# Kernel tuning notes

Hardware: AMD Instinct MI355X
Metric: run time of the kernel (lower is better)

Reference implementation:

```python
import jax, jax.numpy as jnp
import numpy as np

# Model dims (match init_kwargs)
B, S = 2, 2048          # batch, seq_len
H = 1024                # hidden_size
D = 2048                # expert_hidden_dim
E = 8                   # num_experts
K = 2                   # num_experts_per_tok (top_k)


def setup_inputs() -> dict:
    key = jax.random.key(0)
    k_x, k_g, k_w1, k_w2 = jax.random.split(key, 4)
    x = jax.random.normal(k_x, (B, S, H), jnp.float32)
    # router gate: Linear(H, E, bias=False)
    gate_w = jax.random.normal(k_g, (H, E), jnp.float32) / jnp.sqrt(H).astype(jnp.float32)
    # per-expert FFN params stacked on leading expert axis
    W1 = jax.random.normal(k_w1, (E, H, D), jnp.float32) / jnp.sqrt(H).astype(jnp.float32)
    b1 = jnp.zeros((E, D), jnp.float32)
    W2 = jax.random.normal(k_w2, (E, D, H), jnp.float32) / jnp.sqrt(D).astype(jnp.float32)
    b2 = jnp.zeros((E, H), jnp.float32)
    return {"x": x, "gate_w": gate_w, "W1": W1, "b1": b1, "W2": W2, "b2": b2}


def reference(x, gate_w, W1, b1, W2, b2):
    # --- router ---
    logits = jnp.einsum('bsh,he->bse', x, gate_w)            # [B,S,E]
    probs = jax.nn.softmax(logits, axis=-1)                  # [B,S,E]
    topk_p, idx = jax.lax.top_k(probs, K)                    # [B,S,K] each
    topk_p = topk_p / topk_p.sum(axis=-1, keepdims=True)     # renormalize over top-k
    one_hot = jax.nn.one_hot(idx, E, dtype=probs.dtype)      # [B,S,K,E]
    # combine weight per (token, expert); topk indices are distinct so this
    # equals the original's masked-sum of router_probs_flat * expert_mask
    combine = jnp.einsum('bske,bsk->bse', one_hot, topk_p)   # [B,S,E]

    # --- aux load-balancing loss (faithful to original reductions) ---
    tokens_per_expert = one_hot.sum(axis=-2).mean(axis=0)    # [S,E]
    avg_prob_per_expert = probs.mean(axis=(0, 1))            # [E]
    aux_loss = E * (tokens_per_expert * avg_prob_per_expert).sum()

    # --- experts: dense-equivalent of gather-FFN-scatter (tokens with
    # combine weight 0 contribute 0, matching the masked loop) ---
    out = jnp.zeros_like(x)
    for e in range(E):  # fixed small loop over structurally distinct experts
        h = jax.nn.gelu(jnp.einsum('bsh,hd->bsd', x, W1[e]) + b1[e], approximate=False)
        out = out + combine[..., e:e + 1] * (jnp.einsum('bsd,dh->bsh', h, W2[e]) + b2[e])
    return out, aux_loss
```

## Files before the change

### kernel.cpp

```cpp
#include <hip/hip_runtime.h>
#include <hip/hip_bf16.h>

#define NTOK 4096
#define HD   1024
#define DD   2048
#define NE   8
#define SLOTS (2*NTOK)
#define SLOTS_PAD (SLOTS + 128)

typedef unsigned short u16;
typedef unsigned int   u32;
typedef __attribute__((ext_vector_type(8))) __bf16 bf16x8;
typedef __attribute__((ext_vector_type(4))) float  f32x4;

__device__ __forceinline__ float bf2f(u16 u) {
    u32 v = ((u32)u) << 16;
    return __uint_as_float(v);
}
__device__ __forceinline__ u16 f2bf(float f) {
    __hip_bfloat16 h = __float2bfloat16(f);
    return *reinterpret_cast<u16*>(&h);
}

__device__ __forceinline__ void gload_lds16(const void* g, void* l) {
    __builtin_amdgcn_global_load_lds(
        (__attribute__((address_space(1))) void*)g,
        (__attribute__((address_space(3))) void*)l,
        16, 0, 0);
}

__global__ __launch_bounds__(256) void cvt2_k(
        const float* __restrict__ W1, const float* __restrict__ W2,
        u16* __restrict__ W1t, u16* __restrict__ W2t) {
    int z = blockIdx.z;
    const float* src; u16* dst; int R, C;
    if (z < NE) { src = W1 + (size_t)z * HD * DD;        dst = W1t + (size_t)z * HD * DD;        R = HD; C = DD; }
    else        { src = W2 + (size_t)(z - NE) * DD * HD; dst = W2t + (size_t)(z - NE) * DD * HD; R = DD; C = HD; }
    int tcols = C >> 6;
    int r0 = (blockIdx.x / tcols) * 64;
    int c0 = (blockIdx.x % tcols) * 64;

    __shared__ u16 tile[64][68];
    int tid = threadIdx.x;
    int rr  = tid >> 4;
    int cc4 = (tid & 15) * 4;
#pragma unroll
    for (int j = 0; j < 4; ++j) {
        int r = rr + j * 16;
        float4 v = *reinterpret_cast<const float4*>(src + (size_t)(r0 + r) * C + c0 + cc4);
        tile[r][cc4 + 0] = f2bf(v.x); tile[r][cc4 + 1] = f2bf(v.y);
        tile[r][cc4 + 2] = f2bf(v.z); tile[r][cc4 + 3] = f2bf(v.w);
    }
    __syncthreads();
    int cc = tid >> 3, sl = tid & 7;
#pragma unroll
    for (int p = 0; p < 2; ++p) {
        int c = p * 32 + cc;
        u16 tmp[8];
#pragma unroll
        for (int k = 0; k < 8; ++k) tmp[k] = tile[sl * 8 + k][c];
        *reinterpret_cast<uint4*>(dst + (size_t)(c0 + c) * R + r0 + sl * 8) =
            *reinterpret_cast<uint4*>(tmp);
    }
}

__global__ __launch_bounds__(256) void router_k(
        const float* __restrict__ x, const float* __restrict__ gw,
        u16* __restrict__ xb,
        int* __restrict__ counts, float* __restrict__ sum_probs,
        int* __restrict__ tk_idx, float* __restrict__ tk_w) {
    __shared__ int   bcnt[NE];
    __shared__ float bprob[NE];
    int tid = threadIdx.x;
    if (tid < NE) { bcnt[tid] = 0; bprob[tid] = 0.f; }
    __syncthreads();

    int gtid = blockIdx.x * 256 + tid;
    int t    = gtid >> 6;
    int lane = gtid & 63;

    float acc[NE] = {0.f,0.f,0.f,0.f,0.f,0.f,0.f,0.f};
    const float* xr = x + (size_t)t * HD;
    u16* xbr = xb + (size_t)t * HD;
#pragma unroll
    for (int i = 0; i < HD / 64; ++i) {
        int h = lane + i * 64;
        float xv = xr[h];
        xbr[h] = f2bf(xv);
        const float4* g = reinterpret_cast<const float4*>(gw + (size_t)h * NE);
        float4 g0 = g[0], g1 = g[1];
        acc[0] = fmaf(xv, g0.x, acc[0]); acc[1] = fmaf(xv, g0.y, acc[1]);
        acc[2] = fmaf(xv, g0.z, acc[2]); acc[3] = fmaf(xv, g0.w, acc[3]);
        acc[4] = fmaf(xv, g1.x, acc[4]); acc[5] = fmaf(xv, g1.y, acc[5]);
        acc[6] = fmaf(xv, g1.z, acc[6]); acc[7] = fmaf(xv, g1.w, acc[7]);
    }
#pragma unroll
    for (int off = 32; off >= 1; off >>= 1) {
#pragma unroll
        for (int e = 0; e < NE; ++e) acc[e] += __shfl_xor(acc[e], off);
    }
    float m = acc[0];
#pragma unroll
    for (int e = 1; e < NE; ++e) m = fmaxf(m, acc[e]);
    float p[NE]; float s = 0.f;
#pragma unroll
    for (int e = 0; e < NE; ++e) { p[e] = expf(acc[e] - m); s += p[e]; }
    float inv = 1.f / s;

    int i1 = 0; float v1 = p[0];
#pragma unroll
    for (int e = 1; e < NE; ++e) if (p[e] > v1) { v1 = p[e]; i1 = e; }
    int i2 = -1; float v2 = -1.f;
#pragma unroll
    for (int e = 0; e < NE; ++e) if (e != i1 && p[e] > v2) { v2 = p[e]; i2 = e; }
    float wsum = v1 + v2;

    if (lane < NE) atomicAdd(&bprob[lane], p[lane] * inv);
    if (lane == 0) {
        atomicAdd(&bcnt[i1], 1);
        atomicAdd(&bcnt[i2], 1);
        tk_idx[2 * t]     = i1;  tk_idx[2 * t + 1] = i2;
        tk_w[2 * t]       = v1 / wsum;
        tk_w[2 * t + 1]   = v2 / wsum;
    }
    __syncthreads();
    if (tid < NE) {
        if (bcnt[tid]) atomicAdd(&counts[tid], bcnt[tid]);
        atomicAdd(&sum_probs[tid], bprob[tid]);
    }
}

__global__ __launch_bounds__(256) void scatter_k(
        const int* __restrict__ tk_idx, const int* __restrict__ counts,
        int* __restrict__ cursor, int* __restrict__ slot_tok,
        int* __restrict__ inv_slot, int* __restrict__ offsets) {
    __shared__ int off[NE];
    if (threadIdx.x == 0) {
        int o = 0;
        for (int e = 0; e < NE; ++e) { off[e] = o; o += counts[e]; }
        if (blockIdx.x == 0)
            for (int e = 0; e < NE; ++e) offsets[e] = off[e];
    }
    __syncthreads();
    int t = blockIdx.x * 256 + threadIdx.x;
    if (t >= NTOK) return;
#pragma unroll
    for (int k = 0; k < 2; ++k) {
        int e = tk_idx[2 * t + k];
        int pos = atomicAdd(&cursor[e], 1);
        int s = off[e] + pos;
        slot_tok[s] = t;
        inv_slot[2 * t + k] = s;
    }
}

template<int KD, bool GATHER, bool GELU>
__global__ __launch_bounds__(256) void gemm_dense_k(
        const u16* __restrict__ A,
        const u16* __restrict__ Bt,
        const float* __restrict__ bias,
        const int* __restrict__ counts, const int* __restrict__ offsets,
        const int* __restrict__ slot_tok,
        u16* __restrict__ outb, int ND) {
    int mb = blockIdx.y;
    int e = -1, m0 = 0, accb = 0;
#pragma unroll
    for (int ee = 0; ee < NE; ++ee) {
        int nb = (counts[ee] + 127) >> 7;
        if (e < 0 && mb < accb + nb) { e = ee; m0 = (mb - accb) * 128; }
        accb += nb;
    }
    if (e < 0) return;
    int cnt = counts[e], base = offsets[e];
    int n0 = blockIdx.x * 128;

    __shared__ u16 As[128 * 64];
    __shared__ u16 Bs[128 * 64];
    __shared__ int ids[128];

    int tid  = threadIdx.x;
    int lane = tid & 63;
    int w    = tid >> 6;
    int wr   = w >> 1, wc = w & 1;
    int lrow = lane & 15, khi = lane >> 4;

    if constexpr (GATHER) {
        if (tid < 128) ids[tid] = (m0 + tid < cnt) ? slot_tok[base + m0 + tid] : 0;
    }
    __syncthreads();

    const u16* Bte = Bt + (size_t)e * (size_t)ND * KD;
    int srow = tid >> 3;
    int sslot = tid & 7;

    const u16 *gA[4], *gB[4];
#pragma unroll
    for (int j = 0; j < 4; ++j) {
        int r = j * 32 + srow;
        size_t gr;
        if constexpr (GATHER) gr = (size_t)ids[r];
        else                  gr = (size_t)(base + m0 + r);
        gA[j] = A   + gr * KD                + ((sslot ^ (r & 7)) << 3);
        gB[j] = Bte + (size_t)(n0 + r) * KD  + ((sslot ^ (r & 7)) << 3);
    }

    f32x4 acc[4][4];
#pragma unroll
    for (int m = 0; m < 4; ++m)
#pragma unroll
        for (int n = 0; n < 4; ++n) acc[m][n] = {0.f, 0.f, 0.f, 0.f};

    constexpr int NK = KD / 64;
#pragma unroll 1
    for (int t = 0; t < NK; ++t) {
#pragma unroll
        for (int j = 0; j < 4; ++j) {
            gload_lds16(gA[j] + t * 64, (char*)As + j * 4096 + tid * 16);
            gload_lds16(gB[j] + t * 64, (char*)Bs + j * 4096 + tid * 16);
        }
        __syncthreads();
#pragma unroll
        for (int ks = 0; ks < 2; ++ks) {
            int slot = ks * 4 + khi;
            bf16x8 af[4], bv[4];
#pragma unroll
            for (int m = 0; m < 4; ++m) {
                int r = wr * 64 + m * 16 + lrow;
                af[m] = *reinterpret_cast<const bf16x8*>(
                    &As[r * 64 + ((slot ^ (r & 7)) << 3)]);
            }
#pragma unroll
            for (int n = 0; n < 4; ++n) {
                int r = wc * 64 + n * 16 + lrow;
                bv[n] = *reinterpret_cast<const bf16x8*>(
                    &Bs[r * 64 + ((slot ^ (r & 7)) << 3)]);
            }
            __builtin_amdgcn_s_setprio(1);
#pragma unroll
            for (int m = 0; m < 4; ++m)
#pragma unroll
                for (int n = 0; n < 4; ++n)
                    acc[m][n] = __builtin_amdgcn_mfma_f32_16x16x32_bf16(
                        af[m], bv[n], acc[m][n], 0, 0, 0);
            __builtin_amdgcn_s_setprio(0);
        }
        __syncthreads();
    }

    constexpr int PST = 72;
    u16* patch = As + w * 16 * PST;
    float bvals[4];
    if constexpr (GELU) {
#pragma unroll
        for (int n = 0; n < 4; ++n)
            bvals[n] = bias[(size_t)e * ND + n0 + wc * 64 + n * 16 + lrow];
    }
#pragma unroll
    for (int m = 0; m < 4; ++m) {
#pragma unroll
        for (int n = 0; n < 4; ++n)
#pragma unroll
            for (int i = 0; i < 4; ++i) {
                float v = acc[m][n][i];
                if constexpr (GELU) {
                    v += bvals[n];
                    v = 0.5f * v * (1.f + erff(v * 0.70710678118654752f));
                }
                patch[(khi * 4 + i) * PST + n * 16 + lrow] = f2bf(v);
            }
        __syncthreads();
        int prow = lane >> 3, sl = lane & 7;
#pragma unroll
        for (int p = 0; p < 2; ++p) {
            int row  = p * 8 + prow;
            uint4 q = *reinterpret_cast<const uint4*>(&patch[row * PST + sl * 8]);
            int grow = m0 + wr * 64 + m * 16 + row;
            if (grow < cnt)
                *reinterpret_cast<uint4*>(
                    outb + (size_t)(base + grow) * ND + n0 + wc * 64 + sl * 8) = q;
        }
        __syncthreads();
    }
}

__global__ __launch_bounds__(256) void combine_k(
        const int* __restrict__ tk_idx, const float* __restrict__ tk_w,
        const int* __restrict__ inv_slot, const u16* __restrict__ ybuf,
        const float* __restrict__ b2, float* __restrict__ out) {
    int gtid = blockIdx.x * 256 + threadIdx.x;
    int t = gtid >> 6;
    int lane = gtid & 63;
    int e0 = tk_idx[2 * t], e1 = tk_idx[2 * t + 1];
    float w0 = tk_w[2 * t], w1 = tk_w[2 * t + 1];
    int s0 = inv_slot[2 * t], s1 = inv_slot[2 * t + 1];

#pragma unroll
    for (int i = 0; i < 2; ++i) {
        int c = lane * 8 + i * 512;
        uint4 q0 = *reinterpret_cast<const uint4*>(ybuf + (size_t)s0 * HD + c);
        uint4 q1 = *reinterpret_cast<const uint4*>(ybuf + (size_t)s1 * HD + c);
        float y0[8] = {bf2f((u16)(q0.x&0xffff)), bf2f((u16)(q0.x>>16)),
                       bf2f((u16)(q0.y&0xffff)), bf2f((u16)(q0.y>>16)),
                       bf2f((u16)(q0.z&0xffff)), bf2f((u16)(q0.z>>16)),
                       bf2f((u16)(q0.w&0xffff)), bf2f((u16)(q0.w>>16))};
        float y1[8] = {bf2f((u16)(q1.x&0xffff)), bf2f((u16)(q1.x>>16)),
                       bf2f((u16)(q1.y&0xffff)), bf2f((u16)(q1.y>>16)),
                       bf2f((u16)(q1.z&0xffff)), bf2f((u16)(q1.z>>16)),
                       bf2f((u16)(q1.w&0xffff)), bf2f((u16)(q1.w>>16))};
        float r[8];
#pragma unroll
        for (int j = 0; j < 8; ++j) {
            float v0 = y0[j] + b2[e0 * HD + c + j];
            float v1 = y1[j] + b2[e1 * HD + c + j];
            r[j] = w0 * v0 + w1 * v1;
        }
        float* op = out + (size_t)t * HD + c;
        *reinterpret_cast<float4*>(op)     = make_float4(r[0], r[1], r[2], r[3]);
        *reinterpret_cast<float4*>(op + 4) = make_float4(r[4], r[5], r[6], r[7]);
    }
}

__global__ void finalize_k(const int* __restrict__ counts,
                           const float* __restrict__ sum_probs,
                           float* __restrict__ out_aux) {
    if (threadIdx.x == 0) {
        double s = 0.0;
        for (int e = 0; e < NE; ++e) s += (double)counts[e] * (double)sum_probs[e];
        out_aux[0] = (float)(s * (8.0 / (2.0 * (double)NTOK)));
    }
}

extern "C" void kernel_launch(void* const* d_in, const int* in_sizes, int n_in,
                              void* d_out, int out_size, void* d_ws, size_t ws_size,
                              hipStream_t stream) {
    const float* x   = (const float*)d_in[0];
    const float* gw  = (const float*)d_in[1];
    const float* W1  = (const float*)d_in[2];
    const float* b1  = (const float*)d_in[3];
    const float* W2  = (const float*)d_in[4];
    const float* b2  = (const float*)d_in[5];
    float* out = (float*)d_out;

    char* ws = (char*)d_ws;
    int*   counts    = (int*)(ws + 0);
    int*   cursor    = (int*)(ws + 32);
    int*   offsets   = (int*)(ws + 64);
    float* sum_probs = (float*)(ws + 128);
    int*   tk_idx    = (int*)(ws + 512);
    float* tk_w      = (float*)(ws + 33280);
    int*   slot_tok  = (int*)(ws + 66048);
    int*   inv_slot  = (int*)(ws + 98816);
    u16*   xb        = (u16*)(ws + 131584);
    u16*   W1t       = (u16*)(ws + 8520192);
    u16*   W2t       = (u16*)(ws + 42074624);
    u16*   hbuf      = (u16*)(ws + 75629056);
    u16*   ybuf      = W1t;

    hipMemsetAsync(ws, 0, 512, stream);

    cvt2_k<<<dim3(512, 1, 2 * NE), 256, 0, stream>>>(W1, W2, W1t, W2t);
    router_k<<<NTOK / 4, 256, 0, stream>>>(x, gw, xb, counts, sum_probs, tk_idx, tk_w);
    scatter_k<<<NTOK / 256, 256, 0, stream>>>(tk_idx, counts, cursor,
                                              slot_tok, inv_slot, offsets);

    gemm_dense_k<HD, true, true><<<dim3(DD / 128, 72, 1), 256, 0, stream>>>(
        xb, W1t, b1, counts, offsets, slot_tok, hbuf, DD);
    gemm_dense_k<DD, false, false><<<dim3(HD / 128, 72, 1), 256, 0, stream>>>(
        hbuf, W2t, nullptr, counts, offsets, slot_tok, ybuf, HD);

    combine_k<<<NTOK / 4, 256, 0, stream>>>(tk_idx, tk_w, inv_slot, ybuf, b2, out);
    finalize_k<<<1, 64, 0, stream>>>(counts, sum_probs, out + (size_t)NTOK * HD);
}
```

Before: 220.9 us.

## Rewrite expert GEMM as 256x256 tile, 8-wave double-buffered pipelined kernel

Replaces the 128x128 single-buffered grouped GEMM with a 256x256 tile kernel using 8 waves and a double-buffered LDS ring. Global-to-LDS loads for the next k-tile are interleaved with four quadrant MFMA phases under explicit vmcnt/lgkmcnt waits and barriers. This aims to hide memory latency and raise data reuse per loaded tile. In exchange it uses 128KB of LDS, fewer and larger blocks (more padding waste per expert), and carries fragile hand-tuned wait counts.

```diff
diff --git a/kernel.cpp b/kernel.cpp
--- a/kernel.cpp
+++ b/kernel.cpp
@@ -6,12 +6,19 @@
 #define DD   2048
 #define NE   8
 #define SLOTS (2*NTOK)
-#define SLOTS_PAD (SLOTS + 128)
+#define SLOTS_PAD (SLOTS + 256)
 
 typedef unsigned short u16;
 typedef unsigned int   u32;
 typedef __attribute__((ext_vector_type(8))) __bf16 bf16x8;
 typedef __attribute__((ext_vector_type(4))) float  f32x4;
+
+#define WAITV(N) asm volatile("s_waitcnt vmcnt(" #N ")" ::: "memory")
+#define LGKM0()  asm volatile("s_waitcnt lgkmcnt(0)" ::: "memory")
+#define BAR()    __builtin_amdgcn_s_barrier()
+#define SCHEDB() __builtin_amdgcn_sched_barrier(0)
+
+template<int V> struct IC { static constexpr int value = V; };
 
 __device__ __forceinline__ float bf2f(u16 u) {
     u32 v = ((u32)u) << 16;
@@ -155,37 +162,39 @@
 }
 
 template<int KD, bool GATHER, bool GELU>
-__global__ __launch_bounds__(256) void gemm_dense_k(
+__global__ __launch_bounds__(512, 2) void gemm8_k(
         const u16* __restrict__ A,
         const u16* __restrict__ Bt,
         const float* __restrict__ bias,
         const int* __restrict__ counts, const int* __restrict__ offsets,
         const int* __restrict__ slot_tok,
         u16* __restrict__ outb, int ND) {
+    constexpr int NK = KD / 64;
+
     int mb = blockIdx.y;
     int e = -1, m0 = 0, accb = 0;
 #pragma unroll
     for (int ee = 0; ee < NE; ++ee) {
-        int nb = (counts[ee] + 127) >> 7;
-        if (e < 0 && mb < accb + nb) { e = ee; m0 = (mb - accb) * 128; }
+        int nb = (counts[ee] + 255) >> 8;
+        if (e < 0 && mb < accb + nb) { e = ee; m0 = (mb - accb) * 256; }
         accb += nb;
     }
     if (e < 0) return;
     int cnt = counts[e], base = offsets[e];
-    int n0 = blockIdx.x * 128;
-
-    __shared__ u16 As[128 * 64];
-    __shared__ u16 Bs[128 * 64];
-    __shared__ int ids[128];
+    int n0 = blockIdx.x * 256;
+
+    __shared__ u16 smem[65536];
+    __shared__ int ids[256];
 
     int tid  = threadIdx.x;
     int lane = tid & 63;
     int w    = tid >> 6;
-    int wr   = w >> 1, wc = w & 1;
+    int wrr  = w >> 2, wcc = w & 3;
     int lrow = lane & 15, khi = lane >> 4;
 
     if constexpr (GATHER) {
-        if (tid < 128) ids[tid] = (m0 + tid < cnt) ? slot_tok[base + m0 + tid] : 0;
+        for (int i = tid; i < 256; i += 512)
+            ids[i] = (m0 + i < cnt) ? slot_tok[base + m0 + i] : 0;
     }
     __syncthreads();
 
@@ -193,93 +202,159 @@
     int srow = tid >> 3;
     int sslot = tid & 7;
 
-    const u16 *gA[4], *gB[4];
-#pragma unroll
-    for (int j = 0; j < 4; ++j) {
-        int r = j * 32 + srow;
-        size_t gr;
-        if constexpr (GATHER) gr = (size_t)ids[r];
-        else                  gr = (size_t)(base + m0 + r);
-        gA[j] = A   + gr * KD                + ((sslot ^ (r & 7)) << 3);
-        gB[j] = Bte + (size_t)(n0 + r) * KD  + ((sslot ^ (r & 7)) << 3);
-    }
-
-    f32x4 acc[4][4];
-#pragma unroll
-    for (int m = 0; m < 4; ++m)
+    const u16 *pA[2][2], *pB[2][2];
+#pragma unroll
+    for (int h = 0; h < 2; ++h)
+#pragma unroll
+        for (int j = 0; j < 2; ++j) {
+            int r = j * 64 + srow;
+            int R = h * 128 + r;
+            int swz = (sslot ^ (r & 7)) << 3;
+            if constexpr (GATHER) pA[h][j] = A + (size_t)ids[R] * KD + swz;
+            else                  pA[h][j] = A + (size_t)(base + m0 + R) * KD + swz;
+            pB[h][j] = Bte + (size_t)(n0 + R) * KD + swz;
+        }
+
+    auto stageA = [&](int d, int h, int kt) {
+        u16* b = smem + (d * 2 + h) * 8192 + tid * 8;
+        gload_lds16(pA[h][0] + kt * 64, b);
+        gload_lds16(pA[h][1] + kt * 64, b + 4096);
+    };
+    auto stageB = [&](int d, int h, int kt) {
+        u16* b = smem + 32768 + (d * 2 + h) * 8192 + tid * 8;
+        gload_lds16(pB[h][0] + kt * 64, b);
+        gload_lds16(pB[h][1] + kt * 64, b + 4096);
+    };
+
+    bf16x8 afr[4][2];
+    bf16x8 bvr[2][2][2];
+
+    auto ldsA = [&](int d, int mh) {
+        const u16* Rg = smem + (d * 2 + mh) * 8192;
+#pragma unroll
+        for (int m = 0; m < 4; ++m) {
+            int rr = wrr * 64 + m * 16 + lrow;
+#pragma unroll
+            for (int ks = 0; ks < 2; ++ks) {
+                int slot = ks * 4 + khi;
+                afr[m][ks] = *reinterpret_cast<const bf16x8*>(
+                    &Rg[rr * 64 + ((slot ^ (rr & 7)) << 3)]);
+            }
+        }
+    };
+    auto ldsB = [&](int d, auto NHc) {
+        constexpr int nh = decltype(NHc)::value;
+        const u16* Rg = smem + 32768 + (d * 2 + nh) * 8192;
+#pragma unroll
+        for (int fn = 0; fn < 2; ++fn) {
+            int cc = wcc * 32 + fn * 16 + lrow;
+#pragma unroll
+            for (int ks = 0; ks < 2; ++ks) {
+                int slot = ks * 4 + khi;
+                bvr[nh][fn][ks] = *reinterpret_cast<const bf16x8*>(
+                    &Rg[cc * 64 + ((slot ^ (cc & 7)) << 3)]);
+            }
+        }
+    };
+
+    f32x4 acc[8][4];
+#pragma unroll
+    for (int m = 0; m < 8; ++m)
 #pragma unroll
         for (int n = 0; n < 4; ++n) acc[m][n] = {0.f, 0.f, 0.f, 0.f};
 
-    constexpr int NK = KD / 64;
+    auto mfmaQ = [&](auto MHc, auto NHc) {
+        constexpr int mh = decltype(MHc)::value;
+        constexpr int nh = decltype(NHc)::value;
+        __builtin_amdgcn_s_setprio(1);
+#pragma unroll
+        for (int ks = 0; ks < 2; ++ks)
+#pragma unroll
+            for (int m = 0; m < 4; ++m)
+#pragma unroll
+                for (int fn = 0; fn < 2; ++fn)
+                    acc[mh * 4 + m][nh * 2 + fn] =
+                        __builtin_amdgcn_mfma_f32_16x16x32_bf16(
+                            afr[m][ks], bvr[nh][fn][ks],
+                            acc[mh * 4 + m][nh * 2 + fn], 0, 0, 0);
+        __builtin_amdgcn_s_setprio(0);
+    };
+
+    stageA(0, 0, 0); stageB(0, 1, 0); stageB(0, 0, 0);
+    stageA(0, 1, 0); stageA(1, 0, 1); stageB(1, 1, 1);
+    WAITV(6);
+    BAR();
+
 #pragma unroll 1
-    for (int t = 0; t < NK; ++t) {
-#pragma unroll
-        for (int j = 0; j < 4; ++j) {
-            gload_lds16(gA[j] + t * 64, (char*)As + j * 4096 + tid * 16);
-            gload_lds16(gB[j] + t * 64, (char*)Bs + j * 4096 + tid * 16);
-        }
-        __syncthreads();
-#pragma unroll
-        for (int ks = 0; ks < 2; ++ks) {
-            int slot = ks * 4 + khi;
-            bf16x8 af[4], bv[4];
-#pragma unroll
-            for (int m = 0; m < 4; ++m) {
-                int r = wr * 64 + m * 16 + lrow;
-                af[m] = *reinterpret_cast<const bf16x8*>(
-                    &As[r * 64 + ((slot ^ (r & 7)) << 3)]);
-            }
-#pragma unroll
-            for (int n = 0; n < 4; ++n) {
-                int r = wc * 64 + n * 16 + lrow;
-                bv[n] = *reinterpret_cast<const bf16x8*>(
-                    &Bs[r * 64 + ((slot ^ (r & 7)) << 3)]);
-            }
-            __builtin_amdgcn_s_setprio(1);
-#pragma unroll
-            for (int m = 0; m < 4; ++m)
-#pragma unroll
-                for (int n = 0; n < 4; ++n)
-                    acc[m][n] = __builtin_amdgcn_mfma_f32_16x16x32_bf16(
-                        af[m], bv[n], acc[m][n], 0, 0, 0);
-            __builtin_amdgcn_s_setprio(0);
-        }
-        __syncthreads();
-    }
-
-    constexpr int PST = 72;
-    u16* patch = As + w * 16 * PST;
+    for (int kt = 0; kt <= NK - 3; ++kt) {
+        int d = kt & 1;
+        ldsA(d, 0); ldsB(d, IC<0>{});
+        stageB(d ^ 1, 0, kt + 1);
+        BAR(); LGKM0(); SCHEDB();
+        mfmaQ(IC<0>{}, IC<0>{});
+        BAR();
+        ldsB(d, IC<1>{});
+        stageA(d ^ 1, 1, kt + 1);
+        WAITV(8);
+        BAR(); LGKM0(); SCHEDB();
+        mfmaQ(IC<0>{}, IC<1>{});
+        BAR();
+        ldsA(d, 1);
+        stageA(d, 0, kt + 2);
+        BAR(); LGKM0(); SCHEDB();
+        mfmaQ(IC<1>{}, IC<1>{});
+        BAR();
+        stageB(d, 1, kt + 2);
+        WAITV(6);
+        BAR(); SCHEDB();
+        mfmaQ(IC<1>{}, IC<0>{});
+        BAR();
+    }
+    WAITV(0); BAR();
+#pragma unroll 1
+    for (int kt = NK - 2; kt < NK; ++kt) {
+        int d = kt & 1;
+        ldsA(d, 0); ldsB(d, IC<0>{}); LGKM0(); SCHEDB();
+        mfmaQ(IC<0>{}, IC<0>{});
+        ldsB(d, IC<1>{}); LGKM0(); SCHEDB();
+        mfmaQ(IC<0>{}, IC<1>{});
+        ldsA(d, 1); LGKM0(); SCHEDB();
+        mfmaQ(IC<1>{}, IC<1>{});
+        mfmaQ(IC<1>{}, IC<0>{});
+    }
+    BAR();
+
+    u16* patch = smem + w * (16 * 72);
     float bvals[4];
     if constexpr (GELU) {
 #pragma unroll
-        for (int n = 0; n < 4; ++n)
-            bvals[n] = bias[(size_t)e * ND + n0 + wc * 64 + n * 16 + lrow];
-    }
-#pragma unroll
-    for (int m = 0; m < 4; ++m) {
-#pragma unroll
-        for (int n = 0; n < 4; ++n)
+        for (int n4 = 0; n4 < 4; ++n4)
+            bvals[n4] = bias[(size_t)e * ND + n0 + (n4 >> 1) * 128 + wcc * 32 +
+                             (n4 & 1) * 16 + lrow];
+    }
+#pragma unroll
+    for (int m8 = 0; m8 < 8; ++m8) {
+#pragma unroll
+        for (int n4 = 0; n4 < 4; ++n4)
 #pragma unroll
             for (int i = 0; i < 4; ++i) {
-                float v = acc[m][n][i];
+                float v = acc[m8][n4][i];
                 if constexpr (GELU) {
-                    v += bvals[n];
+                    v += bvals[n4];
                     v = 0.5f * v * (1.f + erff(v * 0.70710678118654752f));
                 }
-                patch[(khi * 4 + i) * PST + n * 16 + lrow] = f2bf(v);
+                patch[(khi * 4 + i) * 72 + n4 * 16 + lrow] = f2bf(v);
             }
-        __syncthreads();
-        int prow = lane >> 3, sl = lane & 7;
 #pragma unroll
         for (int p = 0; p < 2; ++p) {
-            int row  = p * 8 + prow;
-            uint4 q = *reinterpret_cast<const uint4*>(&patch[row * PST + sl * 8]);
-            int grow = m0 + wr * 64 + m * 16 + row;
+            int idx = p * 64 + lane;
+            int row = idx >> 3, sl = idx & 7;
+            uint4 q = *reinterpret_cast<const uint4*>(&patch[row * 72 + sl * 8]);
+            int grow = m0 + (m8 >> 2) * 128 + wrr * 64 + (m8 & 3) * 16 + row;
+            int gcol = n0 + (sl >> 2) * 128 + wcc * 32 + ((sl >> 1) & 1) * 16 + (sl & 1) * 8;
             if (grow < cnt)
-                *reinterpret_cast<uint4*>(
-                    outb + (size_t)(base + grow) * ND + n0 + wc * 64 + sl * 8) = q;
+                *reinterpret_cast<uint4*>(outb + (size_t)(base + grow) * ND + gcol) = q;
         }
-        __syncthreads();
     }
 }
 
@@ -363,9 +438,9 @@
     scatter_k<<<NTOK / 256, 256, 0, stream>>>(tk_idx, counts, cursor,
                                               slot_tok, inv_slot, offsets);
 
-    gemm_dense_k<HD, true, true><<<dim3(DD / 128, 72, 1), 256, 0, stream>>>(
+    gemm8_k<HD, true, true><<<dim3(DD / 256, 40, 1), 512, 0, stream>>>(
         xb, W1t, b1, counts, offsets, slot_tok, hbuf, DD);
-    gemm_dense_k<DD, false, false><<<dim3(HD / 128, 72, 1), 256, 0, stream>>>(
+    gemm8_k<DD, false, false><<<dim3(HD / 256, 40, 1), 512, 0, stream>>>(
         hbuf, W2t, nullptr, counts, offsets, slot_tok, ybuf, HD);
 
     combine_k<<<NTOK / 4, 256, 0, stream>>>(tk_idx, tk_w, inv_slot, ybuf, b2, out);
```

New measurement: 253.4 us. +14.7%, slower.
